# Performance work log

Hardware: AMD Instinct MI355X
Metric: run time of the kernel (lower is better)

## Reference

```python
import jax, jax.numpy as jnp
import numpy as np

SPATIAL_SHAPES = [(160, 160), (80, 80), (40, 40)]
D_MODEL = 256
N_HEADS = 8
N_LEVELS = 3
N_POINTS = 4
B = 1
SEQ = sum(h * w for h, w in SPATIAL_SHAPES)  # 33600


def setup_inputs() -> dict:
    key = jax.random.key(0)
    ks = jax.random.split(key, 10)
    f = jax.random.normal
    return {
        "hidden_states": f(ks[0], (B, SEQ, D_MODEL), jnp.float32),
        "encoder_hidden_states": f(ks[1], (B, SEQ, D_MODEL), jnp.float32),
        "position_embeddings": f(ks[2], (B, SEQ, D_MODEL), jnp.float32),
        "reference_points": jax.random.uniform(ks[3], (B, SEQ, N_LEVELS, 2), jnp.float32),
        "Wv": f(ks[4], (D_MODEL, D_MODEL), jnp.float32) * 0.02,
        "bv": jnp.zeros((D_MODEL,), jnp.float32),
        "Ws": f(ks[5], (N_HEADS * N_LEVELS * N_POINTS * 2, D_MODEL), jnp.float32) * 0.02,
        "bs": f(ks[6], (N_HEADS * N_LEVELS * N_POINTS * 2,), jnp.float32) * 2.0,
        "Wa": f(ks[7], (N_HEADS * N_LEVELS * N_POINTS, D_MODEL), jnp.float32) * 0.02,
        "ba": jnp.zeros((N_HEADS * N_LEVELS * N_POINTS,), jnp.float32),
        "Wo": f(ks[8], (D_MODEL, D_MODEL), jnp.float32) * 0.02,
        "bo": jnp.zeros((D_MODEL,), jnp.float32),
    }


def grid_sample_bilinear(img, grid):
    """torch.nn.functional.grid_sample, mode='bilinear', padding_mode='zeros', align_corners=False.
    img: [N, C, Hi, Wi]; grid: [N, Hg, Wg, 2] with (x, y) in [-1, 1]. Returns [N, C, Hg, Wg]."""
    N, C, Hi, Wi = img.shape
    x = (grid[..., 0] + 1.0) * (Wi * 0.5) - 0.5  # unnormalized pixel coords
    y = (grid[..., 1] + 1.0) * (Hi * 0.5) - 0.5
    x0f = jnp.floor(x)
    y0f = jnp.floor(y)
    x0 = x0f.astype(jnp.int32)
    y0 = y0f.astype(jnp.int32)
    wx1 = x - x0f
    wy1 = y - y0f
    imgc = jnp.transpose(img, (0, 2, 3, 1))  # [N, Hi, Wi, C]
    n_idx = jnp.arange(N)[:, None, None]

    def tap(xi, yi, w):
        valid = (xi >= 0) & (xi < Wi) & (yi >= 0) & (yi < Hi)
        xc = jnp.clip(xi, 0, Wi - 1)
        yc = jnp.clip(yi, 0, Hi - 1)
        v = imgc[n_idx, yc, xc]  # [N, Hg, Wg, C]
        return v * (w * valid.astype(img.dtype))[..., None]

    out = (tap(x0, y0, (1.0 - wx1) * (1.0 - wy1))
           + tap(x0 + 1, y0, wx1 * (1.0 - wy1))
           + tap(x0, y0 + 1, (1.0 - wx1) * wy1)
           + tap(x0 + 1, y0 + 1, wx1 * wy1))
    return jnp.transpose(out, (0, 3, 1, 2))  # [N, C, Hg, Wg]


def reference(hidden_states, encoder_hidden_states, position_embeddings, reference_points,
              Wv, bv, Ws, bs, Wa, ba, Wo, bo):
    hd = D_MODEL // N_HEADS
    LP = N_LEVELS * N_POINTS
    Q = SEQ

    hs = hidden_states + position_embeddings  # [B, Q, D]
    value = (encoder_hidden_states @ Wv.T + bv).reshape(B, SEQ, N_HEADS, hd)
    offsets = (hs @ Ws.T + bs).reshape(B * Q, N_HEADS, LP, 2)
    attn = jax.nn.softmax((hs @ Wa.T + ba).reshape(B, Q, N_HEADS, LP), axis=-1)

    # offset normalizer: [w, h] per level, broadcast over points
    norm = jnp.array([[w, h] for (h, w) in SPATIAL_SHAPES], jnp.float32)  # [L, 2]
    norm = jnp.broadcast_to(norm[:, None, :], (N_LEVELS, N_POINTS, 2)).reshape(1, 1, LP, 2)
    rp = reference_points.reshape(-1, N_LEVELS, 1, 2)
    rp = jnp.broadcast_to(rp, (B * Q, N_LEVELS, N_POINTS, 2)).reshape(B * Q, 1, LP, 2)
    loc = rp + offsets / norm                # [BQ, H, LP, 2]
    grids = 2.0 * loc - 1.0

    attn_t = jnp.transpose(attn, (0, 2, 1, 3)).reshape(B * N_HEADS, 1, Q, LP)

    sampled = []
    start = 0
    for lvl, (h, w) in enumerate(SPATIAL_SHAPES):
        v = value[:, start:start + h * w].reshape(B, h * w, N_HEADS * hd)
        v = jnp.transpose(v, (0, 2, 1)).reshape(B * N_HEADS, hd, h, w)
        g = jnp.transpose(grids[:, :, lvl * N_POINTS:(lvl + 1) * N_POINTS], (1, 0, 2, 3))  # [H, BQ, P, 2] (B=1)
        sampled.append(grid_sample_bilinear(v, g))  # [B*H, hd, Q, P]
        start += h * w

    out = (jnp.concatenate(sampled, axis=-1) * attn_t).sum(-1)  # [B*H, hd, Q]
    out = jnp.transpose(out.reshape(B, N_HEADS * hd, Q), (0, 2, 1))  # [B, Q, D]
    output = out @ Wo.T + bo
    return output, attn
```

## Files before the change

kernel.cpp:

```cpp
#include <hip/hip_runtime.h>
#include <math.h>

#define QSEQ 33600

typedef __attribute__((ext_vector_type(8))) short short8;
typedef __attribute__((ext_vector_type(4))) float floatx4;
typedef unsigned short ushort_t;

static __device__ __forceinline__ ushort_t f2bf(float f) {
  unsigned u = __float_as_uint(f);
  return (ushort_t)((u + 0x7FFF + ((u >> 16) & 1)) >> 16);
}

static __device__ __forceinline__ void gload_lds16(const void* g, void* l) {
  __builtin_amdgcn_global_load_lds((__attribute__((address_space(1))) void*)g,
                                   (__attribute__((address_space(3))) void*)l, 16, 0, 0);
}

template <int ASRC, int MODE>
static __device__ __forceinline__ void gemm_body(
    const int bx, const int by,
    const float* __restrict__ A1, const float* __restrict__ A2,
    const ushort_t* __restrict__ Ab,
    const float* __restrict__ B1, const float* __restrict__ B2, const int bsplit,
    const float* __restrict__ b1, const float* __restrict__ b2,
    void* __restrict__ C1, float* __restrict__ C2, const int N,
    ushort_t* smem) {
  ushort_t* As = smem;
  ushort_t* Bs = smem + 6144;

  const int tid = threadIdx.x;
  const int m0 = by * 96;
  const int n0 = bx * 128;
  const int wv = tid >> 6, lane = tid & 63;
  const int wm = wv >> 1, wn = wv & 1;
  const int l16 = lane & 15, quad = lane >> 4;
  const int l8 = l16 & 7;

  const float* gAf[3];
  const float* gAf2[3];
  const ushort_t* gAb[3];
  ushort_t* lA[3];
#pragma unroll
  for (int i = 0; i < 3; ++i) {
    const int c = tid + i * 256;
    const int row = c >> 3, s = c & 7;
    if (ASRC == 0) {
      gAb[i] = Ab + (size_t)(m0 + row) * 256 + ((s ^ (row & 7)) * 8);
      lA[i] = As + (wv * 64 + i * 256) * 8;
    } else {
      gAf[i] = A1 + (size_t)(m0 + row) * 256 + s * 8;
      if (ASRC == 2) gAf2[i] = A2 + (size_t)(m0 + row) * 256 + s * 8;
      lA[i] = As + row * 64 + (s ^ (row & 7)) * 8;
    }
  }
  const float* gBf[4];
  ushort_t* lBf[4];
#pragma unroll
  for (int j = 0; j < 4; ++j) {
    const int c = tid + j * 256;
    const int row = c >> 3, s = c & 7;
    const int grow = n0 + row;
    const float* bsrc;
    int r2;
    if (grow < bsplit) {
      bsrc = B1;
      r2 = grow;
    } else {
      bsrc = B2;
      r2 = grow - bsplit;
      const int rmax = N - bsplit - 1;
      if (r2 > rmax) r2 = rmax;
    }
    gBf[j] = bsrc + (size_t)r2 * 256 + s * 8;
    lBf[j] = Bs + row * 64 + (s ^ (row & 7)) * 8;
  }

  floatx4 acc[3][4];
#pragma unroll
  for (int i = 0; i < 3; ++i)
#pragma unroll
    for (int j = 0; j < 4; ++j) acc[i][j] = (floatx4)(0.f);

  for (int k0 = 0; k0 < 256; k0 += 64) {
    if (ASRC == 0) {
#pragma unroll
      for (int i = 0; i < 3; ++i) gload_lds16(gAb[i] + k0, lA[i]);
    } else {
#pragma unroll
      for (int i = 0; i < 3; ++i) {
        const float4 x0 = *(const float4*)(gAf[i] + k0);
        const float4 x1 = *(const float4*)(gAf[i] + k0 + 4);
        float v[8] = {x0.x, x0.y, x0.z, x0.w, x1.x, x1.y, x1.z, x1.w};
        if (ASRC == 2) {
          const float4 y0 = *(const float4*)(gAf2[i] + k0);
          const float4 y1 = *(const float4*)(gAf2[i] + k0 + 4);
          v[0] += y0.x; v[1] += y0.y; v[2] += y0.z; v[3] += y0.w;
          v[4] += y1.x; v[5] += y1.y; v[6] += y1.z; v[7] += y1.w;
        }
        ushort_t t[8];
#pragma unroll
        for (int e = 0; e < 8; ++e) t[e] = f2bf(v[e]);
        *(short8*)lA[i] = *(const short8*)t;
      }
    }
#pragma unroll
    for (int j = 0; j < 4; ++j) {
      const float4 x0 = *(const float4*)(gBf[j] + k0);
      const float4 x1 = *(const float4*)(gBf[j] + k0 + 4);
      ushort_t t[8] = {f2bf(x0.x), f2bf(x0.y), f2bf(x0.z), f2bf(x0.w),
                       f2bf(x1.x), f2bf(x1.y), f2bf(x1.z), f2bf(x1.w)};
      *(short8*)lBf[j] = *(const short8*)t;
    }
    __syncthreads();

#pragma unroll
    for (int k32 = 0; k32 < 2; ++k32) {
      const int cx = ((k32 * 4 + quad) ^ l8) * 8;
      short8 a[3], b[4];
#pragma unroll
      for (int mi = 0; mi < 3; ++mi)
        a[mi] = *(const short8*)&As[(wm * 48 + mi * 16 + l16) * 64 + cx];
#pragma unroll
      for (int ni = 0; ni < 4; ++ni)
        b[ni] = *(const short8*)&Bs[(wn * 64 + ni * 16 + l16) * 64 + cx];
#pragma unroll
      for (int mi = 0; mi < 3; ++mi)
#pragma unroll
        for (int ni = 0; ni < 4; ++ni)
          acc[mi][ni] = __builtin_amdgcn_mfma_f32_16x16x32_bf16(a[mi], b[ni], acc[mi][ni], 0, 0, 0);
    }
    __syncthreads();
  }

  if (MODE == 0) {
    float* C = (float*)C1;
#pragma unroll
    for (int ni = 0; ni < 4; ++ni) {
      const int col = n0 + wn * 64 + ni * 16 + l16;
      const float bia = b1[col];
#pragma unroll
      for (int mi = 0; mi < 3; ++mi) {
        const int rr = m0 + wm * 48 + mi * 16 + quad * 4;
#pragma unroll
        for (int r = 0; r < 4; ++r)
          C[(size_t)(rr + r) * N + col] = acc[mi][ni][r] + bia;
      }
    }
  } else if (MODE == 1) {
    ushort_t* C = (ushort_t*)C1;
#pragma unroll
    for (int ni = 0; ni < 4; ++ni) {
      const int col = n0 + wn * 64 + ni * 16 + l16;
      const float bia = b1[col];
      const int h = col >> 5, ch = col & 31;
#pragma unroll
      for (int mi = 0; mi < 3; ++mi) {
        const int rr = m0 + wm * 48 + mi * 16 + quad * 4;
#pragma unroll
        for (int r = 0; r < 4; ++r)
          C[((size_t)h * QSEQ + rr + r) * 32 + ch] = f2bf(acc[mi][ni][r] + bia);
      }
    }
  } else {
    float* smf = (float*)smem;
#pragma unroll
    for (int ni = 0; ni < 4; ++ni) {
      const int col = n0 + wn * 64 + ni * 16 + l16;
      if (col < 96) {
        const float bia = b1[col];
#pragma unroll
        for (int mi = 0; mi < 3; ++mi) {
          const int lr = wm * 48 + mi * 16 + quad * 4;
#pragma unroll
          for (int r = 0; r < 4; ++r)
            smf[(lr + r) * 96 + col] = acc[mi][ni][r] + bia;
        }
      } else if (col < 288) {
        const float bia = b2[col - 96];
#pragma unroll
        for (int mi = 0; mi < 3; ++mi) {
          const int rr = m0 + wm * 48 + mi * 16 + quad * 4;
#pragma unroll
          for (int r = 0; r < 4; ++r)
            C2[(size_t)(rr + r) * 192 + (col - 96)] = acc[mi][ni][r] + bia;
        }
      }
    }
    __syncthreads();
    if (bx == 0) {
      float* C = (float*)C1;
#pragma unroll
      for (int p = 0; p < 3; ++p) {
        const int task = tid + p * 256;
        const int row = task >> 3, hh = task & 7;
        float v[12];
        float mx = -1e30f;
#pragma unroll
        for (int i = 0; i < 12; ++i) {
          v[i] = smf[row * 96 + hh * 12 + i];
          mx = fmaxf(mx, v[i]);
        }
        float s = 0.f;
#pragma unroll
        for (int i = 0; i < 12; ++i) {
          v[i] = __expf(v[i] - mx);
          s += v[i];
        }
        const float inv = 1.f / s;
        float4 o[3];
#pragma unroll
        for (int i = 0; i < 3; ++i) {
          o[i].x = v[i * 4 + 0] * inv;
          o[i].y = v[i * 4 + 1] * inv;
          o[i].z = v[i * 4 + 2] * inv;
          o[i].w = v[i * 4 + 3] * inv;
        }
        float4* dst = (float4*)&C[(size_t)(m0 + row) * 96 + hh * 12];
        dst[0] = o[0];
        dst[1] = o[1];
        dst[2] = o[2];
      }
    }
  }
}

__global__ __launch_bounds__(256) void pre_gemms(
    const float* __restrict__ ehs, const float* __restrict__ hidden,
    const float* __restrict__ pos,
    const float* __restrict__ Wv, const float* __restrict__ bv,
    const float* __restrict__ Wa, const float* __restrict__ ba,
    const float* __restrict__ Ws, const float* __restrict__ bs,
    ushort_t* __restrict__ value, float* __restrict__ attn,
    float* __restrict__ sp) {
  extern __shared__ ushort_t smem[];
  if (blockIdx.x < 2)
    gemm_body<1, 1>(blockIdx.x, blockIdx.y, ehs, nullptr, nullptr,
                    Wv, Wv, 1 << 30, bv, nullptr, value, nullptr, 256, smem);
  else
    gemm_body<2, 2>(blockIdx.x - 2, blockIdx.y, hidden, pos, nullptr,
                    Wa, Ws, 96, ba, bs, attn, sp, 288, smem);
}

__global__ __launch_bounds__(256) void out_gemm(
    const ushort_t* __restrict__ samp, const float* __restrict__ Wo,
    const float* __restrict__ bo, float* __restrict__ out) {
  extern __shared__ ushort_t smem[];
  gemm_body<0, 0>(blockIdx.x, blockIdx.y, nullptr, nullptr, samp,
                  Wo, Wo, 1 << 30, bo, nullptr, out, nullptr, 256, smem);
}

__global__ __launch_bounds__(256) void msda_sample_kernel(
    const ushort_t* __restrict__ value,
    const float* __restrict__ sp,
    const float* __restrict__ attn,
    const float* __restrict__ refp,
    ushort_t* __restrict__ outp) {
  __shared__ unsigned wtab[32 * 100];
  const int tid = threadIdx.x;
  const int h = blockIdx.x & 7;
  const int qbase = (blockIdx.x >> 3) * 32;

#pragma unroll
  for (int pass = 0; pass < 2; ++pass) {
    const int it = tid + pass * 256;
    if (it < 384) {
      const int tq = it / 12;
      const int pt = it - tq * 12;
      const int q = qbase + tq;
      const int lvl = pt >> 2;
      const int S = lvl == 0 ? 160 : (lvl == 1 ? 80 : 40);
      const int base = lvl == 0 ? 0 : (lvl == 1 ? 25600 : 32000);

      const float a = attn[q * 96 + h * 12 + pt];
      const float2 off = *(const float2*)&sp[q * 192 + h * 24 + pt * 2];
      const float2 rp = *(const float2*)&refp[q * 6 + lvl * 2];

      const float x = fmaf(rp.x, (float)S, off.x) - 0.5f;
      const float y = fmaf(rp.y, (float)S, off.y) - 0.5f;
      const float xf = floorf(x), yf = floorf(y);
      const int x0 = (int)xf, y0 = (int)yf;
      const float wx1 = x - xf, wy1 = y - yf;

      const float wx0z = (x0 >= 0 && x0 < S) ? 1.f - wx1 : 0.f;
      const float wx1z = (x0 + 1 >= 0 && x0 + 1 < S) ? wx1 : 0.f;
      const float wy0z = (y0 >= 0 && y0 < S) ? 1.f - wy1 : 0.f;
      const float wy1z = (y0 + 1 >= 0 && y0 + 1 < S) ? wy1 : 0.f;

      const int x0c = min(max(x0, 0), S - 1);
      const int x1c = min(max(x0 + 1, 0), S - 1);
      const int y0c = min(max(y0, 0), S - 1);
      const int y1c = min(max(y0 + 1, 0), S - 1);

      const int r0 = base + y0c * S, r1 = base + y1c * S;
      uint4 e0, e1;
      e0.x = __float_as_uint(a * wx0z * wy0z);
      e0.y = (unsigned)(r0 + x0c) << 6;
      e0.z = __float_as_uint(a * wx1z * wy0z);
      e0.w = (unsigned)(r0 + x1c) << 6;
      e1.x = __float_as_uint(a * wx0z * wy1z);
      e1.y = (unsigned)(r1 + x0c) << 6;
      e1.z = __float_as_uint(a * wx1z * wy1z);
      e1.w = (unsigned)(r1 + x1c) << 6;
      unsigned* dst = &wtab[tq * 100 + pt * 8];
      *(uint4*)dst = e0;
      *(uint4*)(dst + 4) = e1;
    }
  }
  __syncthreads();

  const int wv = tid >> 6;
  const int qi = (tid >> 3) & 7;
  const int c = tid & 7;
  const int tq = wv * 8 + qi;
  const int q = qbase + tq;
  const unsigned* wt = &wtab[tq * 100];
  const char* vbase = (const char*)value + ((size_t)h * QSEQ) * 64 + c * 8;

  float f0 = 0.f, f1 = 0.f, f2 = 0.f, f3 = 0.f;
#pragma unroll
  for (int r = 0; r < 48; ++r) {
    const uint2 e = *(const uint2*)&wt[r * 2];
    const float w = __uint_as_float(e.x);
    const uint2 v = *(const uint2*)(vbase + e.y);
    f0 = fmaf(__uint_as_float(v.x << 16), w, f0);
    f1 = fmaf(__uint_as_float(v.x & 0xFFFF0000u), w, f1);
    f2 = fmaf(__uint_as_float(v.y << 16), w, f2);
    f3 = fmaf(__uint_as_float(v.y & 0xFFFF0000u), w, f3);
  }

  ushort_t t[4] = {f2bf(f0), f2bf(f1), f2bf(f2), f2bf(f3)};
  *(uint2*)&outp[(size_t)q * 256 + h * 32 + c * 4] = *(const uint2*)t;
}

extern "C" void kernel_launch(void* const* d_in, const int* in_sizes, int n_in,
                              void* d_out, int out_size, void* d_ws, size_t ws_size,
                              hipStream_t stream) {
  const float* hidden = (const float*)d_in[0];
  const float* ehs    = (const float*)d_in[1];
  const float* pos    = (const float*)d_in[2];
  const float* refp   = (const float*)d_in[3];
  const float* Wv = (const float*)d_in[4];
  const float* bv = (const float*)d_in[5];
  const float* Ws = (const float*)d_in[6];
  const float* bs = (const float*)d_in[7];
  const float* Wa = (const float*)d_in[8];
  const float* ba = (const float*)d_in[9];
  const float* Wo = (const float*)d_in[10];
  const float* bo = (const float*)d_in[11];

  float* out  = (float*)d_out;
  float* attn = out + (size_t)QSEQ * 256;

  char* ws = (char*)d_ws;
  ushort_t* ws_value = (ushort_t*)ws;
  ushort_t* ws_outp  = ws_value + (size_t)QSEQ * 256;
  float* ws_sp = (float*)(ws_outp + (size_t)QSEQ * 256);

  dim3 blk(256);

  pre_gemms<<<dim3(5, 350), blk, 36864, stream>>>(
      ehs, hidden, pos, Wv, bv, Wa, ba, Ws, bs, ws_value, attn, ws_sp);
  msda_sample_kernel<<<dim3((QSEQ / 32) * 8), blk, 0, stream>>>(
      ws_value, ws_sp, attn, refp, ws_outp);
  out_gemm<<<dim3(2, 350), blk, 28672, stream>>>(ws_outp, Wo, bo, out);
}
```

Baseline: 269.0 us.

## Double-buffer GEMM LDS tiles and prefetch next K slice into registers

The shared GEMM body now uses two LDS buffers. It issues the global loads (or direct-to-LDS DMA) for the next 64-wide K slice before running the MFMAs on the current one, then converts and stores that slice to the other buffer. This removes one barrier per iteration and overlaps global latency with compute. The cost is doubled LDS per block (57 KB), more live registers for the prefetched float4s, and launch_bounds of (256,2), which may limit occupancy or cause spills.

```diff
diff --git a/kernel.cpp b/kernel.cpp
--- a/kernel.cpp
+++ b/kernel.cpp
@@ -26,9 +26,6 @@
     const float* __restrict__ b1, const float* __restrict__ b2,
     void* __restrict__ C1, float* __restrict__ C2, const int N,
     ushort_t* smem) {
-  ushort_t* As = smem;
-  ushort_t* Bs = smem + 6144;
-
   const int tid = threadIdx.x;
   const int m0 = by * 96;
   const int n0 = bx * 128;
@@ -40,22 +37,22 @@
   const float* gAf[3];
   const float* gAf2[3];
   const ushort_t* gAb[3];
-  ushort_t* lA[3];
+  int lAoff[3];
 #pragma unroll
   for (int i = 0; i < 3; ++i) {
     const int c = tid + i * 256;
     const int row = c >> 3, s = c & 7;
     if (ASRC == 0) {
       gAb[i] = Ab + (size_t)(m0 + row) * 256 + ((s ^ (row & 7)) * 8);
-      lA[i] = As + (wv * 64 + i * 256) * 8;
+      lAoff[i] = (wv * 64 + i * 256) * 8;
     } else {
       gAf[i] = A1 + (size_t)(m0 + row) * 256 + s * 8;
       if (ASRC == 2) gAf2[i] = A2 + (size_t)(m0 + row) * 256 + s * 8;
-      lA[i] = As + row * 64 + (s ^ (row & 7)) * 8;
+      lAoff[i] = row * 64 + (s ^ (row & 7)) * 8;
     }
   }
   const float* gBf[4];
-  ushort_t* lBf[4];
+  int lBoff[4];
 #pragma unroll
   for (int j = 0; j < 4; ++j) {
     const int c = tid + j * 256;
@@ -73,7 +70,7 @@
       if (r2 > rmax) r2 = rmax;
     }
     gBf[j] = bsrc + (size_t)r2 * 256 + s * 8;
-    lBf[j] = Bs + row * 64 + (s ^ (row & 7)) * 8;
+    lBoff[j] = row * 64 + (s ^ (row & 7)) * 8;
   }
 
   floatx4 acc[3][4];
@@ -82,53 +79,94 @@
 #pragma unroll
     for (int j = 0; j < 4; ++j) acc[i][j] = (floatx4)(0.f);
 
-  for (int k0 = 0; k0 < 256; k0 += 64) {
-    if (ASRC == 0) {
-#pragma unroll
-      for (int i = 0; i < 3; ++i) gload_lds16(gAb[i] + k0, lA[i]);
-    } else {
-#pragma unroll
-      for (int i = 0; i < 3; ++i) {
-        const float4 x0 = *(const float4*)(gAf[i] + k0);
-        const float4 x1 = *(const float4*)(gAf[i] + k0 + 4);
-        float v[8] = {x0.x, x0.y, x0.z, x0.w, x1.x, x1.y, x1.z, x1.w};
-        if (ASRC == 2) {
-          const float4 y0 = *(const float4*)(gAf2[i] + k0);
-          const float4 y1 = *(const float4*)(gAf2[i] + k0 + 4);
-          v[0] += y0.x; v[1] += y0.y; v[2] += y0.z; v[3] += y0.w;
-          v[4] += y1.x; v[5] += y1.y; v[6] += y1.z; v[7] += y1.w;
-        }
-        ushort_t t[8];
-#pragma unroll
-        for (int e = 0; e < 8; ++e) t[e] = f2bf(v[e]);
-        *(short8*)lA[i] = *(const short8*)t;
-      }
-    }
+  float4 aX[3], aY[3], aX2[3], aY2[3];
+  float4 bX[4], bY[4];
+
+  auto loadA = [&](int k0) {
+    if (ASRC == 0) return;
+#pragma unroll
+    for (int i = 0; i < 3; ++i) {
+      aX[i] = *(const float4*)(gAf[i] + k0);
+      aY[i] = *(const float4*)(gAf[i] + k0 + 4);
+      if (ASRC == 2) {
+        aX2[i] = *(const float4*)(gAf2[i] + k0);
+        aY2[i] = *(const float4*)(gAf2[i] + k0 + 4);
+      }
+    }
+  };
+  auto loadB = [&](int k0) {
 #pragma unroll
     for (int j = 0; j < 4; ++j) {
-      const float4 x0 = *(const float4*)(gBf[j] + k0);
-      const float4 x1 = *(const float4*)(gBf[j] + k0 + 4);
-      ushort_t t[8] = {f2bf(x0.x), f2bf(x0.y), f2bf(x0.z), f2bf(x0.w),
-                       f2bf(x1.x), f2bf(x1.y), f2bf(x1.z), f2bf(x1.w)};
-      *(short8*)lBf[j] = *(const short8*)t;
-    }
-    __syncthreads();
-
+      bX[j] = *(const float4*)(gBf[j] + k0);
+      bY[j] = *(const float4*)(gBf[j] + k0 + 4);
+    }
+  };
+  auto writeA = [&](ushort_t* AsB) {
+    if (ASRC == 0) return;
+#pragma unroll
+    for (int i = 0; i < 3; ++i) {
+      float v[8] = {aX[i].x, aX[i].y, aX[i].z, aX[i].w,
+                    aY[i].x, aY[i].y, aY[i].z, aY[i].w};
+      if (ASRC == 2) {
+        v[0] += aX2[i].x; v[1] += aX2[i].y; v[2] += aX2[i].z; v[3] += aX2[i].w;
+        v[4] += aY2[i].x; v[5] += aY2[i].y; v[6] += aY2[i].z; v[7] += aY2[i].w;
+      }
+      ushort_t t[8];
+#pragma unroll
+      for (int e = 0; e < 8; ++e) t[e] = f2bf(v[e]);
+      *(short8*)(AsB + lAoff[i]) = *(const short8*)t;
+    }
+  };
+  auto writeB = [&](ushort_t* BsB) {
+#pragma unroll
+    for (int j = 0; j < 4; ++j) {
+      ushort_t t[8] = {f2bf(bX[j].x), f2bf(bX[j].y), f2bf(bX[j].z), f2bf(bX[j].w),
+                       f2bf(bY[j].x), f2bf(bY[j].y), f2bf(bY[j].z), f2bf(bY[j].w)};
+      *(short8*)(BsB + lBoff[j]) = *(const short8*)t;
+    }
+  };
+  auto dmaA = [&](int k0, ushort_t* AsB) {
+#pragma unroll
+    for (int i = 0; i < 3; ++i) gload_lds16(gAb[i] + k0, AsB + lAoff[i]);
+  };
+
+  if (ASRC == 0) dmaA(0, smem);
+  else { loadA(0); }
+  loadB(0);
+  writeA(smem);
+  writeB(smem + 6144);
+  __syncthreads();
+
+#pragma unroll
+  for (int k = 0; k < 4; ++k) {
+    ushort_t* AsC = smem + (k & 1) * 14336;
+    ushort_t* BsC = AsC + 6144;
+    ushort_t* AsN = smem + ((k + 1) & 1) * 14336;
+    ushort_t* BsN = AsN + 6144;
+    if (k < 3) {
+      if (ASRC == 0) dmaA((k + 1) * 64, AsN);
+      else loadA((k + 1) * 64);
+      loadB((k + 1) * 64);
+    }
 #pragma unroll
     for (int k32 = 0; k32 < 2; ++k32) {
       const int cx = ((k32 * 4 + quad) ^ l8) * 8;
       short8 a[3], b[4];
 #pragma unroll
       for (int mi = 0; mi < 3; ++mi)
-        a[mi] = *(const short8*)&As[(wm * 48 + mi * 16 + l16) * 64 + cx];
+        a[mi] = *(const short8*)&AsC[(wm * 48 + mi * 16 + l16) * 64 + cx];
 #pragma unroll
       for (int ni = 0; ni < 4; ++ni)
-        b[ni] = *(const short8*)&Bs[(wn * 64 + ni * 16 + l16) * 64 + cx];
+        b[ni] = *(const short8*)&BsC[(wn * 64 + ni * 16 + l16) * 64 + cx];
 #pragma unroll
       for (int mi = 0; mi < 3; ++mi)
 #pragma unroll
         for (int ni = 0; ni < 4; ++ni)
           acc[mi][ni] = __builtin_amdgcn_mfma_f32_16x16x32_bf16(a[mi], b[ni], acc[mi][ni], 0, 0, 0);
+    }
+    if (k < 3) {
+      writeA(AsN);
+      writeB(BsN);
     }
     __syncthreads();
   }
@@ -225,7 +263,7 @@
   }
 }
 
-__global__ __launch_bounds__(256) void pre_gemms(
+__global__ __launch_bounds__(256, 2) void pre_gemms(
     const float* __restrict__ ehs, const float* __restrict__ hidden,
     const float* __restrict__ pos,
     const float* __restrict__ Wv, const float* __restrict__ bv,
@@ -242,7 +280,7 @@
                     Wa, Ws, 96, ba, bs, attn, sp, 288, smem);
 }
 
-__global__ __launch_bounds__(256) void out_gemm(
+__global__ __launch_bounds__(256, 2) void out_gemm(
     const ushort_t* __restrict__ samp, const float* __restrict__ Wo,
     const float* __restrict__ bo, float* __restrict__ out) {
   extern __shared__ ushort_t smem[];
@@ -359,9 +397,9 @@
 
   dim3 blk(256);
 
-  pre_gemms<<<dim3(5, 350), blk, 36864, stream>>>(
+  pre_gemms<<<dim3(5, 350), blk, 57344, stream>>>(
       ehs, hidden, pos, Wv, bv, Wa, ba, Ws, bs, ws_value, attn, ws_sp);
   msda_sample_kernel<<<dim3((QSEQ / 32) * 8), blk, 0, stream>>>(
       ws_value, ws_sp, attn, refp, ws_outp);
-  out_gemm<<<dim3(2, 350), blk, 28672, stream>>>(ws_outp, Wo, bo, out);
-}
+  out_gemm<<<dim3(2, 350), blk, 57344, stream>>>(ws_outp, Wo, bo, out);
+}
```

New measurement: 269.2 us. No clear change (+0.1%).

## Keep full-K weight tile in LDS, stream A fragments directly to registers

Applied to the files above, without the earlier changes.

The GEMM body now loads the whole 128x256 B (weight) tile into LDS once as bf16, using hardware packed bf16 conversion, and drops the per-K-step LDS staging of A. Each lane reads its A fragments straight from global memory into MFMA registers, which removes three of the four barrier pairs per block. The 2D grids become 1D, with an XCD-aware remap that gives each XCD a contiguous range of tiles for L2 locality, and launch bounds request two blocks per CU. This raises LDS use to 64KB per block and relies on uncoalesced-ish per-lane A loads that no longer share data through LDS. The packed conversion instruction may also round differently from the old manual round-to-nearest-even.

```diff
diff --git a/kernel.cpp b/kernel.cpp
--- a/kernel.cpp
+++ b/kernel.cpp
@@ -12,9 +12,24 @@
   return (ushort_t)((u + 0x7FFF + ((u >> 16) & 1)) >> 16);
 }
 
-static __device__ __forceinline__ void gload_lds16(const void* g, void* l) {
-  __builtin_amdgcn_global_load_lds((__attribute__((address_space(1))) void*)g,
-                                   (__attribute__((address_space(3))) void*)l, 16, 0, 0);
+static __device__ __forceinline__ unsigned pk2bf(float lo, float hi) {
+  unsigned r;
+  asm("v_cvt_pk_bf16_f32 %0, %1, %2" : "=v"(r) : "v"(lo), "v"(hi));
+  return r;
+}
+
+static __device__ __forceinline__ short8 cvt8(const float4 x0, const float4 x1) {
+  union { unsigned u[4]; short8 s; } r;
+  r.u[0] = pk2bf(x0.x, x0.y);
+  r.u[1] = pk2bf(x0.z, x0.w);
+  r.u[2] = pk2bf(x1.x, x1.y);
+  r.u[3] = pk2bf(x1.z, x1.w);
+  return r.s;
+}
+
+static __device__ __forceinline__ float4 add4(float4 a, const float4 b) {
+  a.x += b.x; a.y += b.y; a.z += b.z; a.w += b.w;
+  return a;
 }
 
 template <int ASRC, int MODE>
@@ -26,9 +41,6 @@
     const float* __restrict__ b1, const float* __restrict__ b2,
     void* __restrict__ C1, float* __restrict__ C2, const int N,
     ushort_t* smem) {
-  ushort_t* As = smem;
-  ushort_t* Bs = smem + 6144;
-
   const int tid = threadIdx.x;
   const int m0 = by * 96;
   const int n0 = bx * 128;
@@ -37,29 +49,10 @@
   const int l16 = lane & 15, quad = lane >> 4;
   const int l8 = l16 & 7;
 
-  const float* gAf[3];
-  const float* gAf2[3];
-  const ushort_t* gAb[3];
-  ushort_t* lA[3];
-#pragma unroll
-  for (int i = 0; i < 3; ++i) {
-    const int c = tid + i * 256;
-    const int row = c >> 3, s = c & 7;
-    if (ASRC == 0) {
-      gAb[i] = Ab + (size_t)(m0 + row) * 256 + ((s ^ (row & 7)) * 8);
-      lA[i] = As + (wv * 64 + i * 256) * 8;
-    } else {
-      gAf[i] = A1 + (size_t)(m0 + row) * 256 + s * 8;
-      if (ASRC == 2) gAf2[i] = A2 + (size_t)(m0 + row) * 256 + s * 8;
-      lA[i] = As + row * 64 + (s ^ (row & 7)) * 8;
-    }
-  }
-  const float* gBf[4];
-  ushort_t* lBf[4];
-#pragma unroll
-  for (int j = 0; j < 4; ++j) {
-    const int c = tid + j * 256;
-    const int row = c >> 3, s = c & 7;
+#pragma unroll
+  for (int it = 0; it < 16; ++it) {
+    const int c = tid + it * 256;
+    const int row = c >> 5, kc = c & 31;
     const int grow = n0 + row;
     const float* bsrc;
     int r2;
@@ -72,9 +65,30 @@
       const int rmax = N - bsplit - 1;
       if (r2 > rmax) r2 = rmax;
     }
-    gBf[j] = bsrc + (size_t)r2 * 256 + s * 8;
-    lBf[j] = Bs + row * 64 + (s ^ (row & 7)) * 8;
-  }
+    const float* src = bsrc + (size_t)r2 * 256 + kc * 8;
+    const float4 x0 = *(const float4*)src;
+    const float4 x1 = *(const float4*)(src + 4);
+    const short8 v = cvt8(x0, x1);
+    *(short8*)&smem[(row * 32 + (kc ^ (row & 7))) * 8] = v;
+  }
+  __syncthreads();
+
+  const float* pA[3];
+  const float* pA2[3];
+  const ushort_t* pAb[3];
+#pragma unroll
+  for (int mi = 0; mi < 3; ++mi) {
+    const int rr = m0 + wm * 48 + mi * 16 + l16;
+    if (ASRC == 0) {
+      pAb[mi] = Ab + (size_t)rr * 256 + quad * 8;
+    } else {
+      pA[mi] = A1 + (size_t)rr * 256 + quad * 8;
+      if (ASRC == 2) pA2[mi] = A2 + (size_t)rr * 256 + quad * 8;
+    }
+  }
+  int brow[4];
+#pragma unroll
+  for (int ni = 0; ni < 4; ++ni) brow[ni] = (wn * 64 + ni * 16 + l16) * 256;
 
   floatx4 acc[3][4];
 #pragma unroll
@@ -82,55 +96,33 @@
 #pragma unroll
     for (int j = 0; j < 4; ++j) acc[i][j] = (floatx4)(0.f);
 
-  for (int k0 = 0; k0 < 256; k0 += 64) {
-    if (ASRC == 0) {
-#pragma unroll
-      for (int i = 0; i < 3; ++i) gload_lds16(gAb[i] + k0, lA[i]);
-    } else {
-#pragma unroll
-      for (int i = 0; i < 3; ++i) {
-        const float4 x0 = *(const float4*)(gAf[i] + k0);
-        const float4 x1 = *(const float4*)(gAf[i] + k0 + 4);
-        float v[8] = {x0.x, x0.y, x0.z, x0.w, x1.x, x1.y, x1.z, x1.w};
+#pragma unroll
+  for (int k32 = 0; k32 < 8; ++k32) {
+    short8 a[3], b[4];
+#pragma unroll
+    for (int mi = 0; mi < 3; ++mi) {
+      if (ASRC == 0) {
+        a[mi] = *(const short8*)(pAb[mi] + k32 * 32);
+      } else {
+        float4 x0 = *(const float4*)(pA[mi] + k32 * 32);
+        float4 x1 = *(const float4*)(pA[mi] + k32 * 32 + 4);
         if (ASRC == 2) {
-          const float4 y0 = *(const float4*)(gAf2[i] + k0);
-          const float4 y1 = *(const float4*)(gAf2[i] + k0 + 4);
-          v[0] += y0.x; v[1] += y0.y; v[2] += y0.z; v[3] += y0.w;
-          v[4] += y1.x; v[5] += y1.y; v[6] += y1.z; v[7] += y1.w;
-        }
-        ushort_t t[8];
-#pragma unroll
-        for (int e = 0; e < 8; ++e) t[e] = f2bf(v[e]);
-        *(short8*)lA[i] = *(const short8*)t;
-      }
-    }
-#pragma unroll
-    for (int j = 0; j < 4; ++j) {
-      const float4 x0 = *(const float4*)(gBf[j] + k0);
-      const float4 x1 = *(const float4*)(gBf[j] + k0 + 4);
-      ushort_t t[8] = {f2bf(x0.x), f2bf(x0.y), f2bf(x0.z), f2bf(x0.w),
-                       f2bf(x1.x), f2bf(x1.y), f2bf(x1.z), f2bf(x1.w)};
-      *(short8*)lBf[j] = *(const short8*)t;
-    }
-    __syncthreads();
-
-#pragma unroll
-    for (int k32 = 0; k32 < 2; ++k32) {
-      const int cx = ((k32 * 4 + quad) ^ l8) * 8;
-      short8 a[3], b[4];
-#pragma unroll
-      for (int mi = 0; mi < 3; ++mi)
-        a[mi] = *(const short8*)&As[(wm * 48 + mi * 16 + l16) * 64 + cx];
+          x0 = add4(x0, *(const float4*)(pA2[mi] + k32 * 32));
+          x1 = add4(x1, *(const float4*)(pA2[mi] + k32 * 32 + 4));
+        }
+        a[mi] = cvt8(x0, x1);
+      }
+    }
+#pragma unroll
+    for (int ni = 0; ni < 4; ++ni) {
+      const int slot = ((k32 << 2) | quad) ^ l8;
+      b[ni] = *(const short8*)&smem[brow[ni] + slot * 8];
+    }
+#pragma unroll
+    for (int mi = 0; mi < 3; ++mi)
 #pragma unroll
       for (int ni = 0; ni < 4; ++ni)
-        b[ni] = *(const short8*)&Bs[(wn * 64 + ni * 16 + l16) * 64 + cx];
-#pragma unroll
-      for (int mi = 0; mi < 3; ++mi)
-#pragma unroll
-        for (int ni = 0; ni < 4; ++ni)
-          acc[mi][ni] = __builtin_amdgcn_mfma_f32_16x16x32_bf16(a[mi], b[ni], acc[mi][ni], 0, 0, 0);
-    }
-    __syncthreads();
+        acc[mi][ni] = __builtin_amdgcn_mfma_f32_16x16x32_bf16(a[mi], b[ni], acc[mi][ni], 0, 0, 0);
   }
 
   if (MODE == 0) {
@@ -163,6 +155,7 @@
       }
     }
   } else {
+    __syncthreads();
     float* smf = (float*)smem;
 #pragma unroll
     for (int ni = 0; ni < 4; ++ni) {
@@ -225,7 +218,7 @@
   }
 }
 
-__global__ __launch_bounds__(256) void pre_gemms(
+__global__ __launch_bounds__(256, 2) void pre_gemms(
     const float* __restrict__ ehs, const float* __restrict__ hidden,
     const float* __restrict__ pos,
     const float* __restrict__ Wv, const float* __restrict__ bv,
@@ -234,19 +227,27 @@
     ushort_t* __restrict__ value, float* __restrict__ attn,
     float* __restrict__ sp) {
   extern __shared__ ushort_t smem[];
-  if (blockIdx.x < 2)
-    gemm_body<1, 1>(blockIdx.x, blockIdx.y, ehs, nullptr, nullptr,
+  const int bid = blockIdx.x;
+  const int xcd = bid & 7, idx = bid >> 3;
+  const int work = (xcd < 6 ? xcd * 219 : 1314 + (xcd - 6) * 218) + idx;
+  if (work < 700)
+    gemm_body<1, 1>(work & 1, work >> 1, ehs, nullptr, nullptr,
                     Wv, Wv, 1 << 30, bv, nullptr, value, nullptr, 256, smem);
-  else
-    gemm_body<2, 2>(blockIdx.x - 2, blockIdx.y, hidden, pos, nullptr,
+  else {
+    const int w2 = work - 700;
+    gemm_body<2, 2>(w2 % 3, w2 / 3, hidden, pos, nullptr,
                     Wa, Ws, 96, ba, bs, attn, sp, 288, smem);
-}
-
-__global__ __launch_bounds__(256) void out_gemm(
+  }
+}
+
+__global__ __launch_bounds__(256, 2) void out_gemm(
     const ushort_t* __restrict__ samp, const float* __restrict__ Wo,
     const float* __restrict__ bo, float* __restrict__ out) {
   extern __shared__ ushort_t smem[];
-  gemm_body<0, 0>(blockIdx.x, blockIdx.y, nullptr, nullptr, samp,
+  const int bid = blockIdx.x;
+  const int xcd = bid & 7, idx = bid >> 3;
+  const int work = (xcd < 4 ? xcd * 88 : 352 + (xcd - 4) * 87) + idx;
+  gemm_body<0, 0>(work & 1, work >> 1, nullptr, nullptr, samp,
                   Wo, Wo, 1 << 30, bo, nullptr, out, nullptr, 256, smem);
 }
 
@@ -359,9 +360,9 @@
 
   dim3 blk(256);
 
-  pre_gemms<<<dim3(5, 350), blk, 36864, stream>>>(
+  pre_gemms<<<dim3(1750), blk, 65536, stream>>>(
       ehs, hidden, pos, Wv, bv, Wa, ba, Ws, bs, ws_value, attn, ws_sp);
   msda_sample_kernel<<<dim3((QSEQ / 32) * 8), blk, 0, stream>>>(
       ws_value, ws_sp, attn, refp, ws_outp);
-  out_gemm<<<dim3(2, 350), blk, 28672, stream>>>(ws_outp, Wo, bo, out);
-}
+  out_gemm<<<dim3(700), blk, 65536, stream>>>(ws_outp, Wo, bo, out);
+}
```

Result: slower. 322.2 us (+19.8%).
